# Kernel tuning notes

Measured on AMD Instinct MI355X. Metric: run time of the kernel, lower is better.

The kernel has to match this reference:

```python
import jax, jax.numpy as jnp
import numpy as np


def setup_inputs() -> dict:
    key = jax.random.key(0)
    ks = jax.random.split(key, 9)
    B, F, D = 512, 32, 64
    units = [128, 128, 128]
    inp = {
        "x": jax.random.normal(ks[0], (B, F, D), dtype=jnp.float32),
        "W0": jax.random.normal(ks[1], (units[0], F * F), dtype=jnp.float32) * 0.02,
        "b0": jax.random.normal(ks[2], (units[0],), dtype=jnp.float32) * 0.02,
        "W1": jax.random.normal(ks[3], (units[1], units[0] * F), dtype=jnp.float32) * 0.02,
        "b1": jax.random.normal(ks[4], (units[1],), dtype=jnp.float32) * 0.02,
        "W2": jax.random.normal(ks[5], (units[2], units[1] * F), dtype=jnp.float32) * 0.02,
        "b2": jax.random.normal(ks[6], (units[2],), dtype=jnp.float32) * 0.02,
        "Wout": jax.random.normal(ks[7], (sum(units), 1), dtype=jnp.float32) * 0.02,
        "bout": jax.random.normal(ks[8], (1,), dtype=jnp.float32) * 0.02,
    }
    return inp


def reference(x, W0, b0, W1, b1, W2, b2, Wout, bout):
    # x: [B, F, D]
    B, F, D = x.shape
    x0 = x[:, :, None, :]  # [B, F, 1, D]
    h = x                   # [B, H, D], H starts at F
    outs = []
    for W, b in ((W0, b0), (W1, b1), (W2, b2)):
        # outer product over field dims: [B, F, H, D]
        z = x0 * h[:, None, :, :]
        Bn, Fd, Hd, Dd = z.shape
        z = z.reshape(Bn, Fd * Hd, Dd)  # channels = f*H + h (torch view order)
        # 1x1 Conv1d == matmul over channels: [B, C_in, D] x [C_out, C_in]
        y = jnp.einsum('bcd,oc->bod', z, W) + b[None, :, None]  # [B, U, D]
        h = y
        outs.append(y.sum(axis=2))  # [B, U]
    out = jnp.concatenate(outs, axis=1)       # [B, sum(units)]
    out = jax.nn.relu(out)
    out = out @ Wout + bout                    # [B, 1]
    return jax.nn.sigmoid(out)
```

## Files before the change

kernel.cpp:

```cpp
#include <hip/hip_runtime.h>
#include <math.h>


typedef __attribute__((ext_vector_type(8))) _Float16 f16x8;
typedef __attribute__((ext_vector_type(4))) float f32x4;
typedef __attribute__((ext_vector_type(4))) unsigned short u16x4;

__device__ __forceinline__ unsigned short f2h(float f) {
  union { _Float16 h; unsigned short u; } c; c.h = (_Float16)f; return c.u;
}

__device__ __forceinline__ void gll16(const void* g, void* l) {
  __builtin_amdgcn_global_load_lds(
      (const __attribute__((address_space(1))) unsigned int*)g,
      (__attribute__((address_space(3))) unsigned int*)l, 16, 0, 0);
}

__global__ void repack_w_kernel(const float* __restrict__ W, unsigned short* __restrict__ dst,
                                int H, int nthreads)
{
  const int t = blockIdx.x * 256 + threadIdx.x;
  if (t >= nthreads) return;
  const int K = 32 * H;
  const int idx = t & 511;
  const int c   = t >> 9;
  const int pass = c >> 5, f = c & 31;
  const int mt = idx >> 6, l = idx & 63;
  const int o = mt * 16 + (l & 15);
  const int kcol = f * H + pass * 32 + ((l >> 4) & 3) * 8;
  const float* s = W + (size_t)o * K + kcol;
  u16x4 a, bq;
#pragma unroll
  for (int j = 0; j < 4; ++j) {
    a[j]  = f2h(s[j]);
    bq[j] = f2h(s[4 + j]);
  }
  *(u16x4*)(dst + (size_t)t * 8)     = a;
  *(u16x4*)(dst + (size_t)t * 8 + 4) = bq;
}

#define BODY(FCUR, Ac, CNEXT, Ad)                                               \
  {                                                                             \
    const float sc0 = lx[(FCUR) * 64 +  0 + li];                                \
    const float sc1 = lx[(FCUR) * 64 + 16 + li];                                \
    const float sc2 = lx[(FCUR) * 64 + 32 + li];                                \
    const float sc3 = lx[(FCUR) * 64 + 48 + li];                                \
    f32x4 G0, G1, G2, G3;                                                       \
    __builtin_amdgcn_s_setprio(1);                                              \
    G0 = __builtin_amdgcn_mfma_f32_16x16x32_f16(Ac, Bh[0], zero4, 0, 0, 0);     \
    G1 = __builtin_amdgcn_mfma_f32_16x16x32_f16(Ac, Bh[1], zero4, 0, 0, 0);     \
    G2 = __builtin_amdgcn_mfma_f32_16x16x32_f16(Ac, Bh[2], zero4, 0, 0, 0);     \
    G3 = __builtin_amdgcn_mfma_f32_16x16x32_f16(Ac, Bh[3], zero4, 0, 0, 0);     \
    __builtin_amdgcn_s_setprio(0);                                              \
    {                                                                           \
      size_t cn_ = (size_t)(CNEXT);                                             \
      if (cn_ > (size_t)(NIT - 1)) cn_ = (size_t)(NIT - 1);                     \
      Ad = Abase[cn_ * 512];                                                    \
    }                                                                           \
    Y[0] += G0 * sc0;                                                           \
    Y[1] += G1 * sc1;                                                           \
    Y[2] += G2 * sc2;                                                           \
    Y[3] += G3 * sc3;                                                           \
  }

template<int H, int NPASS, bool FIRST, bool STORE_H>
__global__ __launch_bounds__(512, 4) void cin_mfma_layer(
    const unsigned short* __restrict__ Wimg,
    const float* __restrict__ x,
    const unsigned short* __restrict__ hTin,
    const float* __restrict__ bias,
    unsigned short* __restrict__ hTout,
    float* __restrict__ outs, int col_off)
{
  constexpr int NIT = NPASS * 32;
  __shared__ char lds[8192];
  const int tid = threadIdx.x;
  const int w = tid >> 6, l = tid & 63, g = l >> 4, li = l & 15;
  const int b = blockIdx.x;
  const float* lx = (const float*)lds;

  gll16(x + (size_t)b * 2048 + tid * 4, lds + w * 1024);

  f32x4 Y[4];
#pragma unroll
  for (int nt = 0; nt < 4; ++nt) Y[nt] = (f32x4){0.f, 0.f, 0.f, 0.f};
  const f32x4 zero4 = (f32x4){0.f, 0.f, 0.f, 0.f};
  f16x8 Bh[4];

  asm volatile("s_waitcnt vmcnt(0)" ::: "memory");
  __builtin_amdgcn_s_barrier();

  if constexpr (FIRST) {
#pragma unroll
    for (int nt = 0; nt < 4; ++nt) {
      union { f16x8 v; _Float16 u[8]; } th;
#pragma unroll
      for (int j = 0; j < 8; ++j) {
        const float xv = lx[(g * 8 + j) * 64 + nt * 16 + li];
        th.u[j] = (_Float16)xv;
      }
      Bh[nt] = th.v;
    }
  }

  const f16x8* Abase = (const f16x8*)Wimg + (w * 64 + l);

  f16x8 Aa = Abase[0];
  f16x8 Ab = Abase[512];

  for (int pass = 0; pass < NPASS; ++pass) {
    if constexpr (!FIRST) {
#pragma unroll
      for (int nt = 0; nt < 4; ++nt) {
        const size_t off = (size_t)b * 8192 + (size_t)(nt * 16 + li) * 128
                         + pass * 32 + g * 8;
        Bh[nt] = *(const f16x8*)(hTin + off);
      }
    }
    const int cb = pass * 32;
#pragma unroll 1
    for (int fo = 0; fo < 32; fo += 2) {
      BODY(fo,     Aa, cb + fo + 2, Aa)
      BODY(fo + 1, Ab, cb + fo + 3, Ab)
    }
  }

  const f32x4 bv = *(const f32x4*)(bias + w * 16 + g * 4);
#pragma unroll
  for (int nt = 0; nt < 4; ++nt) Y[nt] += bv;

  if constexpr (STORE_H) {
#pragma unroll
    for (int nt = 0; nt < 4; ++nt) {
      const int d = nt * 16 + li;
      u16x4 ph;
#pragma unroll
      for (int j = 0; j < 4; ++j) ph[j] = f2h(Y[nt][j]);
      const size_t off = (size_t)b * 8192 + (size_t)d * 128 + w * 16 + g * 4;
      *(u16x4*)(hTout + off) = ph;
    }
  }

  {
    f32x4 s = Y[0] + Y[1] + Y[2] + Y[3];
#pragma unroll
    for (int m = 1; m < 16; m <<= 1) {
      s.x += __shfl_xor(s.x, m, 16);
      s.y += __shfl_xor(s.y, m, 16);
      s.z += __shfl_xor(s.z, m, 16);
      s.w += __shfl_xor(s.w, m, 16);
    }
    if (li == 0)
      *(f32x4*)(outs + (size_t)b * 384 + col_off + w * 16 + g * 4) = s;
  }
}

__global__ __launch_bounds__(64) void cin_final_kernel(
    const float* __restrict__ outs, const float* __restrict__ Wout,
    const float* __restrict__ bout, float* __restrict__ out)
{
  const int b = blockIdx.x;
  const int lane = threadIdx.x;
  float p = 0.f;
  for (int j = lane; j < 384; j += 64) {
    float v = outs[(size_t)b * 384 + j];
    v = v > 0.f ? v : 0.f;
    p = fmaf(v, Wout[j], p);
  }
#pragma unroll
  for (int m = 32; m; m >>= 1) p += __shfl_xor(p, m, 64);
  if (lane == 0) {
    const float t = p + bout[0];
    out[b] = 1.f / (1.f + expf(-t));
  }
}

extern "C" void kernel_launch(void* const* d_in, const int* in_sizes, int n_in,
                              void* d_out, int out_size, void* d_ws, size_t ws_size,
                              hipStream_t stream)
{
  const float* x    = (const float*)d_in[0];
  const float* W0   = (const float*)d_in[1];
  const float* b0   = (const float*)d_in[2];
  const float* W1   = (const float*)d_in[3];
  const float* b1   = (const float*)d_in[4];
  const float* W2   = (const float*)d_in[5];
  const float* b2   = (const float*)d_in[6];
  const float* Wout = (const float*)d_in[7];
  const float* bout = (const float*)d_in[8];
  float* out = (float*)d_out;

  char* ws = (char*)d_ws;
  unsigned short* hT1  = (unsigned short*)ws;
  unsigned short* hT2  = (unsigned short*)(ws + (8 << 20));
  float*          outs = (float*)        (ws + (16 << 20));
  unsigned short* Wi0  = (unsigned short*)(ws + (17 << 20));
  unsigned short* Wi1  = (unsigned short*)(ws + (17 << 20) + (1 << 19));
  unsigned short* Wi2  = (unsigned short*)(ws + (17 << 20) + (1 << 19) + (1 << 20));

  repack_w_kernel<<<64,  256, 0, stream>>>(W0, Wi0, 32,  16384);
  repack_w_kernel<<<256, 256, 0, stream>>>(W1, Wi1, 128, 65536);
  repack_w_kernel<<<256, 256, 0, stream>>>(W2, Wi2, 128, 65536);

  cin_mfma_layer<32,  1, true,  true ><<<512, 512, 0, stream>>>(Wi0, x, nullptr, b0, hT1, outs, 0);
  cin_mfma_layer<128, 4, false, true ><<<512, 512, 0, stream>>>(Wi1, x, hT1,    b1, hT2, outs, 128);
  cin_mfma_layer<128, 4, false, false><<<512, 512, 0, stream>>>(Wi2, x, hT2,    b2, nullptr, outs, 256);

  cin_final_kernel<<<512, 64, 0, stream>>>(outs, Wout, bout, out);
}
```

Measured before the change: 114.9 us.

## Merge weight repacks into one launch and fuse final sigmoid into last layer

The three weight-repack launches become a single kernel that picks its source matrix from the block index. The separate final ReLU/linear/sigmoid kernel is folded into the last CIN layer: it reduces its own sums through LDS and reads the earlier layers' sums from a narrower workspace. The A-operand prefetch now uses a running pointer instead of a clamped index, which removes per-iteration address math. In exchange, the last prefetches read past each weight image, so Wi2 is moved to leave slack in the workspace.

```diff
diff --git a/kernel.cpp b/kernel.cpp
--- a/kernel.cpp
+++ b/kernel.cpp
@@ -16,11 +16,16 @@
       (__attribute__((address_space(3))) unsigned int*)l, 16, 0, 0);
 }
 
-__global__ void repack_w_kernel(const float* __restrict__ W, unsigned short* __restrict__ dst,
-                                int H, int nthreads)
+__global__ void repack_w_all(const float* __restrict__ W0q, const float* __restrict__ W1q,
+                             const float* __restrict__ W2q,
+                             unsigned short* __restrict__ D0, unsigned short* __restrict__ D1,
+                             unsigned short* __restrict__ D2)
 {
-  const int t = blockIdx.x * 256 + threadIdx.x;
-  if (t >= nthreads) return;
+  const int blk = blockIdx.x;
+  const float* W; unsigned short* dst; int H, t;
+  if (blk < 64)       { W = W0q; dst = D0; H = 32;  t = blk * 256 + threadIdx.x; }
+  else if (blk < 320) { W = W1q; dst = D1; H = 128; t = (blk - 64) * 256 + threadIdx.x; }
+  else                { W = W2q; dst = D2; H = 128; t = (blk - 320) * 256 + threadIdx.x; }
   const int K = 32 * H;
   const int idx = t & 511;
   const int c   = t >> 9;
@@ -39,12 +44,12 @@
   *(u16x4*)(dst + (size_t)t * 8 + 4) = bq;
 }
 
-#define BODY(FCUR, Ac, CNEXT, Ad)                                               \
+#define BODY(SPOFF, Ac, Ad, Ap)                                                 \
   {                                                                             \
-    const float sc0 = lx[(FCUR) * 64 +  0 + li];                                \
-    const float sc1 = lx[(FCUR) * 64 + 16 + li];                                \
-    const float sc2 = lx[(FCUR) * 64 + 32 + li];                                \
-    const float sc3 = lx[(FCUR) * 64 + 48 + li];                                \
+    const float sc0 = lxp[(SPOFF) +  0 + li];                                   \
+    const float sc1 = lxp[(SPOFF) + 16 + li];                                   \
+    const float sc2 = lxp[(SPOFF) + 32 + li];                                   \
+    const float sc3 = lxp[(SPOFF) + 48 + li];                                   \
     f32x4 G0, G1, G2, G3;                                                       \
     __builtin_amdgcn_s_setprio(1);                                              \
     G0 = __builtin_amdgcn_mfma_f32_16x16x32_f16(Ac, Bh[0], zero4, 0, 0, 0);     \
@@ -52,27 +57,26 @@
     G2 = __builtin_amdgcn_mfma_f32_16x16x32_f16(Ac, Bh[2], zero4, 0, 0, 0);     \
     G3 = __builtin_amdgcn_mfma_f32_16x16x32_f16(Ac, Bh[3], zero4, 0, 0, 0);     \
     __builtin_amdgcn_s_setprio(0);                                              \
-    {                                                                           \
-      size_t cn_ = (size_t)(CNEXT);                                             \
-      if (cn_ > (size_t)(NIT - 1)) cn_ = (size_t)(NIT - 1);                     \
-      Ad = Abase[cn_ * 512];                                                    \
-    }                                                                           \
+    Ad = Ap[0];                                                                 \
+    Ap += 1024;                                                                 \
     Y[0] += G0 * sc0;                                                           \
     Y[1] += G1 * sc1;                                                           \
     Y[2] += G2 * sc2;                                                           \
     Y[3] += G3 * sc3;                                                           \
   }
 
-template<int H, int NPASS, bool FIRST, bool STORE_H>
+template<int H, int NPASS, bool FIRST, bool STORE_H, bool FINAL>
 __global__ __launch_bounds__(512, 4) void cin_mfma_layer(
     const unsigned short* __restrict__ Wimg,
     const float* __restrict__ x,
     const unsigned short* __restrict__ hTin,
     const float* __restrict__ bias,
     unsigned short* __restrict__ hTout,
-    float* __restrict__ outs, int col_off)
+    float* __restrict__ outs, int col_off,
+    const float* __restrict__ Wout,
+    const float* __restrict__ bout,
+    float* __restrict__ out)
 {
-  constexpr int NIT = NPASS * 32;
   __shared__ char lds[8192];
   const int tid = threadIdx.x;
   const int w = tid >> 6, l = tid & 63, g = l >> 4, li = l & 15;
@@ -107,6 +111,8 @@
 
   f16x8 Aa = Abase[0];
   f16x8 Ab = Abase[512];
+  const f16x8* ApA = Abase + 1024;
+  const f16x8* ApB = Abase + 1536;
 
   for (int pass = 0; pass < NPASS; ++pass) {
     if constexpr (!FIRST) {
@@ -117,11 +123,12 @@
         Bh[nt] = *(const f16x8*)(hTin + off);
       }
     }
-    const int cb = pass * 32;
+    const float* lxp = lx;
 #pragma unroll 1
     for (int fo = 0; fo < 32; fo += 2) {
-      BODY(fo,     Aa, cb + fo + 2, Aa)
-      BODY(fo + 1, Ab, cb + fo + 3, Ab)
+      BODY(0,  Aa, Aa, ApA)
+      BODY(64, Ab, Ab, ApB)
+      lxp += 128;
     }
   }
 
@@ -141,37 +148,43 @@
     }
   }
 
-  {
-    f32x4 s = Y[0] + Y[1] + Y[2] + Y[3];
-#pragma unroll
-    for (int m = 1; m < 16; m <<= 1) {
-      s.x += __shfl_xor(s.x, m, 16);
-      s.y += __shfl_xor(s.y, m, 16);
-      s.z += __shfl_xor(s.z, m, 16);
-      s.w += __shfl_xor(s.w, m, 16);
-    }
+  f32x4 s = Y[0] + Y[1] + Y[2] + Y[3];
+#pragma unroll
+  for (int m = 1; m < 16; m <<= 1) {
+    s.x += __shfl_xor(s.x, m, 16);
+    s.y += __shfl_xor(s.y, m, 16);
+    s.z += __shfl_xor(s.z, m, 16);
+    s.w += __shfl_xor(s.w, m, 16);
+  }
+
+  if constexpr (FINAL) {
+    __builtin_amdgcn_s_barrier();
+    float* shs = (float*)lds;
+    if (li == 0) *(f32x4*)(shs + w * 16 + g * 4) = s;
+    __builtin_amdgcn_s_barrier();
+    if (w == 0) {
+      float acc;
+      {
+        float v0 = shs[l];      v0 = v0 > 0.f ? v0 : 0.f;
+        float v1 = shs[l + 64]; v1 = v1 > 0.f ? v1 : 0.f;
+        acc = v0 * Wout[256 + l] + v1 * Wout[320 + l];
+      }
+#pragma unroll
+      for (int q = 0; q < 4; ++q) {
+        float v = outs[(size_t)b * 256 + q * 64 + l];
+        v = v > 0.f ? v : 0.f;
+        acc = fmaf(v, Wout[q * 64 + l], acc);
+      }
+#pragma unroll
+      for (int m = 32; m; m >>= 1) acc += __shfl_xor(acc, m, 64);
+      if (l == 0) {
+        const float t = acc + bout[0];
+        out[b] = 1.f / (1.f + expf(-t));
+      }
+    }
+  } else {
     if (li == 0)
-      *(f32x4*)(outs + (size_t)b * 384 + col_off + w * 16 + g * 4) = s;
-  }
-}
-
-__global__ __launch_bounds__(64) void cin_final_kernel(
-    const float* __restrict__ outs, const float* __restrict__ Wout,
-    const float* __restrict__ bout, float* __restrict__ out)
-{
-  const int b = blockIdx.x;
-  const int lane = threadIdx.x;
-  float p = 0.f;
-  for (int j = lane; j < 384; j += 64) {
-    float v = outs[(size_t)b * 384 + j];
-    v = v > 0.f ? v : 0.f;
-    p = fmaf(v, Wout[j], p);
-  }
-#pragma unroll
-  for (int m = 32; m; m >>= 1) p += __shfl_xor(p, m, 64);
-  if (lane == 0) {
-    const float t = p + bout[0];
-    out[b] = 1.f / (1.f + expf(-t));
+      *(f32x4*)(outs + (size_t)b * 256 + col_off + w * 16 + g * 4) = s;
   }
 }
 
@@ -196,15 +209,14 @@
   float*          outs = (float*)        (ws + (16 << 20));
   unsigned short* Wi0  = (unsigned short*)(ws + (17 << 20));
   unsigned short* Wi1  = (unsigned short*)(ws + (17 << 20) + (1 << 19));
-  unsigned short* Wi2  = (unsigned short*)(ws + (17 << 20) + (1 << 19) + (1 << 20));
-
-  repack_w_kernel<<<64,  256, 0, stream>>>(W0, Wi0, 32,  16384);
-  repack_w_kernel<<<256, 256, 0, stream>>>(W1, Wi1, 128, 65536);
-  repack_w_kernel<<<256, 256, 0, stream>>>(W2, Wi2, 128, 65536);
-
-  cin_mfma_layer<32,  1, true,  true ><<<512, 512, 0, stream>>>(Wi0, x, nullptr, b0, hT1, outs, 0);
-  cin_mfma_layer<128, 4, false, true ><<<512, 512, 0, stream>>>(Wi1, x, hT1,    b1, hT2, outs, 128);
-  cin_mfma_layer<128, 4, false, false><<<512, 512, 0, stream>>>(Wi2, x, hT2,    b2, nullptr, outs, 256);
-
-  cin_final_kernel<<<512, 64, 0, stream>>>(outs, Wout, bout, out);
-}
+  unsigned short* Wi2  = (unsigned short*)(ws + (19 << 20));
+
+  repack_w_all<<<576, 256, 0, stream>>>(W0, W1, W2, Wi0, Wi1, Wi2);
+
+  cin_mfma_layer<32,  1, true,  true,  false><<<512, 512, 0, stream>>>(
+      Wi0, x, nullptr, b0, hT1, outs, 0, nullptr, nullptr, nullptr);
+  cin_mfma_layer<128, 4, false, true,  false><<<512, 512, 0, stream>>>(
+      Wi1, x, hT1, b1, hT2, outs, 128, nullptr, nullptr, nullptr);
+  cin_mfma_layer<128, 4, false, false, true ><<<512, 512, 0, stream>>>(
+      Wi2, x, hT2, b2, nullptr, outs, 0, Wout, bout, out);
+}
```

Result: faster. 106.5 us (-7.4%).
